# Kernel optimization log

Hardware: AMD Instinct MI355X
Metric: run time of the kernel (lower is better)

Reference implementation:

```python
import jax, jax.numpy as jnp
import numpy as np

SEQ, BATCH, D_MODEL, HEADS = 2048, 4, 1024, 16
D_K = D_MODEL // HEADS
SCALE = 1.0 / np.sqrt(D_K).astype(np.float32)


def setup_inputs() -> dict:
    key = jax.random.key(0)
    ks = jax.random.split(key, 12)
    s = 0.02
    inp = {
        "query": jax.random.normal(ks[0], (SEQ, BATCH, D_MODEL), jnp.float32),
        "key": jax.random.normal(ks[1], (SEQ, BATCH, D_MODEL), jnp.float32),
        "value": jax.random.normal(ks[2], (SEQ, BATCH, D_MODEL), jnp.float32),
        # causal mask [seq_q, seq_k, 1]; batch dim broadcasts per prepare_mask
        "mask": jnp.tril(jnp.ones((SEQ, SEQ), jnp.int32))[:, :, None],
        "Wq": jax.random.normal(ks[3], (D_MODEL, D_MODEL), jnp.float32) * s,
        "bq": jnp.zeros((D_MODEL,), jnp.float32),
        "Wk": jax.random.normal(ks[4], (D_MODEL, D_MODEL), jnp.float32) * s,
        "bk": jnp.zeros((D_MODEL,), jnp.float32),
        "Wv": jax.random.normal(ks[5], (D_MODEL, D_MODEL), jnp.float32) * s,
        "bv": jnp.zeros((D_MODEL,), jnp.float32),
        "Wo": jax.random.normal(ks[6], (D_MODEL, D_MODEL), jnp.float32) * s,
        "bo": jnp.zeros((D_MODEL,), jnp.float32),
    }
    return inp


def _heads(x, W, b):
    # [s, b, d_model] -> [s, b, h, d_k]
    y = jnp.einsum('sbd,de->sbe', x, W.T) + b
    return y.reshape(x.shape[0], x.shape[1], HEADS, D_K)


def reference(query, key, value, mask, Wq, bq, Wk, bk, Wv, bv, Wo, bo):
    seq_len, batch_size, _ = query.shape
    q = _heads(query, Wq, bq)
    k = _heads(key, Wk, bk)
    v = _heads(value, Wv, bv)
    # scores [i, j, b, h]
    scores = jnp.einsum('ibhd,jbhd->ijbh', q, k) * SCALE
    m = mask[:, :, :, None]  # [sq, sk, b_or_1, 1]
    scores = jnp.where(m == 0, jnp.float32(-jnp.inf), scores)
    attn = jax.nn.softmax(scores, axis=1)  # softmax over key dim j
    x = jnp.einsum('ijbh,jbhd->ibhd', attn, v)
    x = x.reshape(seq_len, batch_size, D_MODEL)
    return jnp.einsum('sbd,de->sbe', x, Wo.T) + bo
```

## Files before the change

### kernel.cpp

```cpp
#include <hip/hip_runtime.h>
#include <hip/hip_bf16.h>

#define SEQ 2048
#define BATCH 4
#define DM 1024
#define HEADS 16
#define DK 64
#define NBH 64
#define SC_LOG2E (0.125f * 1.4426950408889634f)

typedef unsigned short u16;
typedef __attribute__((ext_vector_type(8))) short bf16x8;
typedef __attribute__((ext_vector_type(4))) float f32x4;

__device__ inline u16 f2bf(float f) {
    unsigned int u = __builtin_bit_cast(unsigned int, f);
    u += 0x7fffu + ((u >> 16) & 1u);
    return (u16)(u >> 16);
}
__device__ inline float fexp2(float x) {
    float r; asm("v_exp_f32 %0, %1" : "=v"(r) : "v"(x)); return r;
}
__device__ inline unsigned pkbf(float a, float b) {
    unsigned r; asm("v_cvt_pk_bf16_f32 %0, %1, %2" : "=v"(r) : "v"(a), "v"(b)); return r;
}

__global__ __launch_bounds__(256)
void conv_w(const float* __restrict__ wq, const float* __restrict__ wk,
            const float* __restrict__ wv, const float* __restrict__ wo,
            u16* __restrict__ ow)
{
    const size_t W8 = (size_t)DM * DM / 8;
    size_t i = (size_t)blockIdx.x * 256 + threadIdx.x;
    int wsel = (int)(i >> 17);
    size_t off = i & (W8 - 1);
    const float* src = wsel == 0 ? wq : wsel == 1 ? wk : wsel == 2 ? wv : wo;
    u16* dst = ow + (size_t)wsel * DM * DM;
    float4 a = ((const float4*)src)[off * 2];
    float4 b = ((const float4*)src)[off * 2 + 1];
    uint4 w;
    w.x = pkbf(a.x, a.y); w.y = pkbf(a.z, a.w);
    w.z = pkbf(b.x, b.y); w.w = pkbf(b.z, b.w);
    *(uint4*)(dst + off * 8) = w;
}

__device__ inline void gstage(const u16* __restrict__ src, u16* dst,
                              int wave, int lane) {
    #pragma unroll
    for (int i = 0; i < 4; ++i) {
        int ci = (i * 4 + wave) * 64 + lane;
        int row = ci >> 3, ch = ci & 7;
        const u16* g = src + (size_t)row * 1024 + ((ch ^ (row & 7)) << 3);
        u16* l = dst + (i * 4 + wave) * 512;
        __builtin_amdgcn_global_load_lds(
            (const __attribute__((address_space(1))) unsigned int*)g,
            (__attribute__((address_space(3))) unsigned int*)l, 16, 0, 0);
    }
}
__device__ inline bf16x8 rdt(const u16* t, int row, int ch) {
    return *(const bf16x8*)(t + row * 64 + ((ch ^ (row & 7)) << 3));
}

__global__ __launch_bounds__(256, 2)
void gemm_bf(const u16* __restrict__ A, const u16* __restrict__ B,
             const float* __restrict__ bias, float* __restrict__ Out)
{
    __shared__ __align__(16) u16 sA[2][128 * 64];
    __shared__ __align__(16) u16 sB[2][128 * 64];
    const int tid  = threadIdx.x;
    const int lane = tid & 63, wave = tid >> 6;
    const int wr = (wave >> 1) * 64, wc = (wave & 1) * 64;
    const int l15 = lane & 15, lg = lane >> 4;
    const int row0 = blockIdx.x * 128, col0 = blockIdx.y * 128;
    const u16* Abase = A + (size_t)row0 * 1024;
    const u16* Bbase = B + (size_t)col0 * 1024;

    f32x4 acc[4][4];
    #pragma unroll
    for (int m = 0; m < 4; ++m)
        #pragma unroll
        for (int n = 0; n < 4; ++n) acc[m][n] = (f32x4){0.f, 0.f, 0.f, 0.f};

    gstage(Abase, sA[0], wave, lane);
    gstage(Bbase, sB[0], wave, lane);
    __syncthreads();

    int cur = 0;
    for (int kt = 0; kt < 16; ++kt) {
        if (kt < 15) {
            gstage(Abase + (kt + 1) * 64, sA[cur ^ 1], wave, lane);
            gstage(Bbase + (kt + 1) * 64, sB[cur ^ 1], wave, lane);
        }
        #pragma unroll
        for (int s = 0; s < 2; ++s) {
            bf16x8 af[4], bf[4];
            #pragma unroll
            for (int m = 0; m < 4; ++m)
                af[m] = rdt(sA[cur], wr + m * 16 + l15, s * 4 + lg);
            #pragma unroll
            for (int n = 0; n < 4; ++n)
                bf[n] = rdt(sB[cur], wc + n * 16 + l15, s * 4 + lg);
            __builtin_amdgcn_s_setprio(1);
            #pragma unroll
            for (int m = 0; m < 4; ++m)
                #pragma unroll
                for (int n = 0; n < 4; ++n)
                    acc[m][n] = __builtin_amdgcn_mfma_f32_16x16x32_bf16(
                        af[m], bf[n], acc[m][n], 0, 0, 0);
            __builtin_amdgcn_s_setprio(0);
        }
        __syncthreads();
        cur ^= 1;
    }
    #pragma unroll
    for (int m = 0; m < 4; ++m)
        #pragma unroll
        for (int n = 0; n < 4; ++n)
            #pragma unroll
            for (int r = 0; r < 4; ++r) {
                int R = row0 + wr + m * 16 + lg * 4 + r;
                int E = col0 + wc + n * 16 + l15;
                Out[(size_t)R * 1024 + E] = acc[m][n][r] + bias[E];
            }
}

__global__ __launch_bounds__(256, 2)
void gemm_qkv(const float* __restrict__ q, const float* __restrict__ k,
              const float* __restrict__ v, const u16* __restrict__ Wbf,
              const float* __restrict__ bq, const float* __restrict__ bk,
              const float* __restrict__ bv,
              u16* __restrict__ Qb, u16* __restrict__ Kb, u16* __restrict__ Vt)
{
    __shared__ __align__(16) u16 sA[2][128 * 64];
    __shared__ __align__(16) u16 sB[2][128 * 64];
    const int g = blockIdx.y >> 3;
    const float* A    = g == 0 ? q  : g == 1 ? k  : v;
    const float* bias = g == 0 ? bq : g == 1 ? bk : bv;
    u16* Out          = g == 0 ? Qb : g == 1 ? Kb : Vt;
    const u16* B = Wbf + (size_t)g * DM * DM;
    const float oscale = g == 0 ? SC_LOG2E : 1.0f;
    const bool vmode = (g == 2);

    const int tid  = threadIdx.x;
    const int lane = tid & 63, wave = tid >> 6;
    const int wr = (wave >> 1) * 64, wc = (wave & 1) * 64;
    const int l15 = lane & 15, lg = lane >> 4;
    const int row0 = blockIdx.x * 128, col0 = (blockIdx.y & 7) * 128;
    const int arow = tid >> 4;
    const int ach  = tid & 15;
    const float* Ag = A + (size_t)(row0 + arow) * 1024 + ach * 4;
    const u16* Bbase = B + (size_t)col0 * 1024;

    f32x4 acc[4][4];
    #pragma unroll
    for (int m = 0; m < 4; ++m)
        #pragma unroll
        for (int n = 0; n < 4; ++n) acc[m][n] = (f32x4){0.f, 0.f, 0.f, 0.f};

    auto loadA = [&](int kt, float4* r) {
        #pragma unroll
        for (int i = 0; i < 8; ++i)
            r[i] = *(const float4*)(Ag + (size_t)i * 16 * 1024 + kt * 64);
    };
    auto writeA = [&](const float4* r, u16* dst) {
        const int c16 = ach >> 1, half = ach & 1;
        #pragma unroll
        for (int i = 0; i < 8; ++i) {
            int row = arow + 16 * i;
            uint2 w;
            w.x = pkbf(r[i].x, r[i].y);
            w.y = pkbf(r[i].z, r[i].w);
            *(uint2*)(dst + row * 64 + ((c16 ^ (row & 7)) << 3) + half * 4) = w;
        }
    };

    {
        float4 a0[8];
        loadA(0, a0);
        gstage(Bbase, sB[0], wave, lane);
        writeA(a0, sA[0]);
    }
    __syncthreads();

    int cur = 0;
    for (int kt = 0; kt < 16; ++kt) {
        float4 an[8];
        const bool pre = (kt < 15);
        if (pre) {
            loadA(kt + 1, an);
            gstage(Bbase + (kt + 1) * 64, sB[cur ^ 1], wave, lane);
        }
        #pragma unroll
        for (int s = 0; s < 2; ++s) {
            bf16x8 af[4], bf[4];
            #pragma unroll
            for (int m = 0; m < 4; ++m)
                af[m] = rdt(sA[cur], wr + m * 16 + l15, s * 4 + lg);
            #pragma unroll
            for (int n = 0; n < 4; ++n)
                bf[n] = rdt(sB[cur], wc + n * 16 + l15, s * 4 + lg);
            __builtin_amdgcn_s_setprio(1);
            #pragma unroll
            for (int m = 0; m < 4; ++m)
                #pragma unroll
                for (int n = 0; n < 4; ++n)
                    acc[m][n] = __builtin_amdgcn_mfma_f32_16x16x32_bf16(
                        af[m], bf[n], acc[m][n], 0, 0, 0);
            __builtin_amdgcn_s_setprio(0);
        }
        if (pre) writeA(an, sA[cur ^ 1]);
        __syncthreads();
        cur ^= 1;
    }

    #pragma unroll
    for (int m = 0; m < 4; ++m)
        #pragma unroll
        for (int n = 0; n < 4; ++n)
            #pragma unroll
            for (int r = 0; r < 4; ++r) {
                int R = row0 + wr + m * 16 + lg * 4 + r;
                int E = col0 + wc + n * 16 + l15;
                float val = (acc[m][n][r] + bias[E]) * oscale;
                int s = R >> 2, b = R & 3, hh = E >> 6, d = E & 63;
                size_t idx = vmode
                    ? ((size_t)(b * HEADS + hh) * DK + d) * SEQ + s
                    : ((size_t)(b * HEADS + hh) * SEQ + s) * DK + d;
                Out[idx] = f2bf(val);
            }
}

__device__ inline void stage_tile(const u16* __restrict__ srcRow0, int srcStride,
                                  u16* tile, int wave, int lane) {
    #pragma unroll
    for (int i = 0; i < 2; ++i) {
        int row = wave * 16 + i * 8 + (lane >> 3);
        int chunk = (lane & 7) ^ (row & 7);
        const u16* g = srcRow0 + (size_t)row * srcStride + chunk * 8;
        u16* l = tile + (wave * 16 + i * 8) * 64;
        __builtin_amdgcn_global_load_lds(
            (const __attribute__((address_space(1))) unsigned int*)g,
            (__attribute__((address_space(3))) unsigned int*)l, 16, 0, 0);
    }
}
__device__ inline bf16x8 tread(const u16* tile, int row, int chunk) {
    return *(const bf16x8*)((const char*)tile + row * 128 + ((chunk ^ (row & 7)) << 4));
}

__global__ __launch_bounds__(256, 4)
void attn_fwd(const u16* __restrict__ Q, const u16* __restrict__ K,
              const u16* __restrict__ V, u16* __restrict__ X)
{
    __shared__ __align__(16) u16 sK[2][4096];
    __shared__ __align__(16) u16 sV[2][4096];
    __shared__ __align__(16) u16 plds[4][16 * 64];

    const int lin = blockIdx.x + 16 * blockIdx.y;
    const int xcd = lin & 7, ii = lin >> 3;
    const int bh  = (ii & 7) | (xcd << 3);
    const int tA  = ii >> 3;
    const int tB  = 31 - tA;
    const int b = bh >> 4, h = bh & 15;
    const int lane = threadIdx.x & 63, wave = threadIdx.x >> 6;
    const int l15 = lane & 15, lg = lane >> 4;
    const int qloc = wave * 16 + l15;
    const int swz = (l15 & 7) << 4;
    const u16* Qh = Q + (size_t)bh * SEQ * DK;
    const u16* Kh = K + (size_t)bh * SEQ * DK;
    const u16* Vh = V + (size_t)bh * SEQ * DK;

    const int qA = tA * 64 + wave * 16, qB = tB * 64 + wave * 16;
    const bf16x8 qfA0 = *(const bf16x8*)&Qh[(size_t)(qA + l15) * DK + lg * 8];
    const bf16x8 qfA1 = *(const bf16x8*)&Qh[(size_t)(qA + l15) * DK + 32 + lg * 8];
    const bf16x8 qfB0 = *(const bf16x8*)&Qh[(size_t)(qB + l15) * DK + lg * 8];
    const bf16x8 qfB1 = *(const bf16x8*)&Qh[(size_t)(qB + l15) * DK + 32 + lg * 8];

    f32x4 oA[4], oB[4];
    #pragma unroll
    for (int n = 0; n < 4; ++n) {
        oA[n] = (f32x4){0.f, 0.f, 0.f, 0.f};
        oB[n] = (f32x4){0.f, 0.f, 0.f, 0.f};
    }
    float lsA = 0.f, lsB = 0.f;
    u16* pw = &plds[wave][0];

    auto compute = [&](const u16* kt, const u16* vt,
                       const bf16x8& q0v, const bf16x8& q1v,
                       f32x4* o, float& ls, bool diag) {
        f32x4 sc[4];
        #pragma unroll
        for (int c = 0; c < 4; ++c) sc[c] = (f32x4){0.f, 0.f, 0.f, 0.f};

        __builtin_amdgcn_s_setprio(1);
        #pragma unroll
        for (int c = 0; c < 4; ++c) {
            bf16x8 k0 = tread(kt, 16 * c + l15, lg);
            bf16x8 k1 = tread(kt, 16 * c + l15, 4 + lg);
            sc[c] = __builtin_amdgcn_mfma_f32_16x16x32_bf16(k0, q0v, sc[c], 0, 0, 0);
            sc[c] = __builtin_amdgcn_mfma_f32_16x16x32_bf16(k1, q1v, sc[c], 0, 0, 0);
        }
        __builtin_amdgcn_s_setprio(0);

        #pragma unroll
        for (int c = 0; c < 4; ++c) {
            float p[4];
            #pragma unroll
            for (int r = 0; r < 4; ++r) {
                float e = fexp2(sc[c][r]);
                if (diag) {
                    int kl = 16 * c + 4 * lg + r;
                    e = (kl <= qloc) ? e : 0.f;
                }
                p[r] = e;
                ls += e;
            }
            uint2 w;
            w.x = pkbf(p[0], p[1]);
            w.y = pkbf(p[2], p[3]);
            *(uint2*)((char*)pw + l15 * 128 + ((32 * c + 8 * lg) ^ swz)) = w;
        }
        asm volatile("s_waitcnt lgkmcnt(0)" ::: "memory");
        __builtin_amdgcn_sched_barrier(0);
        bf16x8 pf0 = *(const bf16x8*)((const char*)pw + l15 * 128 + ((16 * lg) ^ swz));
        bf16x8 pf1 = *(const bf16x8*)((const char*)pw + l15 * 128 + ((64 + 16 * lg) ^ swz));

        __builtin_amdgcn_s_setprio(1);
        #pragma unroll
        for (int n = 0; n < 4; ++n) {
            bf16x8 v0 = tread(vt, 16 * n + l15, lg);
            bf16x8 v1 = tread(vt, 16 * n + l15, 4 + lg);
            o[n] = __builtin_amdgcn_mfma_f32_16x16x32_bf16(pf0, v0, o[n], 0, 0, 0);
            o[n] = __builtin_amdgcn_mfma_f32_16x16x32_bf16(pf1, v1, o[n], 0, 0, 0);
        }
        __builtin_amdgcn_s_setprio(0);
    };

    stage_tile(Kh, DK, sK[0], wave, lane);
    stage_tile(Vh, SEQ, sV[0], wave, lane);
    __syncthreads();

    const int nst = tB + 1;
    int cur = 0;
    for (int blk = 0; blk < nst; ++blk) {
        if (blk + 1 < nst) {
            stage_tile(Kh + (size_t)(blk + 1) * 64 * DK, DK, sK[cur ^ 1], wave, lane);
            stage_tile(Vh + (blk + 1) * 64, SEQ, sV[cur ^ 1], wave, lane);
        }
        if (blk <= tA)
            compute(sK[cur], sV[cur], qfA0, qfA1, oA, lsA, blk == tA);
        compute(sK[cur], sV[cur], qfB0, qfB1, oB, lsB, blk == tB);
        __syncthreads();
        cur ^= 1;
    }

    auto finish = [&](f32x4* o, float ls, int q0) {
        float tot = ls;
        tot += __shfl_xor(tot, 16, 64);
        tot += __shfl_xor(tot, 32, 64);
        float inv[4];
        #pragma unroll
        for (int r = 0; r < 4; ++r)
            inv[r] = 1.0f / __shfl(tot, lg * 4 + r, 64);
        #pragma unroll
        for (int n = 0; n < 4; ++n)
            #pragma unroll
            for (int r = 0; r < 4; ++r) {
                const int i = q0 + lg * 4 + r;
                X[((size_t)i * BATCH + b) * DM + h * DK + 16 * n + l15] =
                    f2bf(o[n][r] * inv[r]);
            }
    };
    finish(oA, lsA, qA);
    finish(oB, lsB, qB);
}

extern "C" void kernel_launch(void* const* d_in, const int* in_sizes, int n_in,
                              void* d_out, int out_size, void* d_ws, size_t ws_size,
                              hipStream_t stream) {
    const float* query = (const float*)d_in[0];
    const float* key   = (const float*)d_in[1];
    const float* value = (const float*)d_in[2];
    const float* Wq = (const float*)d_in[4];
    const float* bq = (const float*)d_in[5];
    const float* Wk = (const float*)d_in[6];
    const float* bk = (const float*)d_in[7];
    const float* Wv = (const float*)d_in[8];
    const float* bv = (const float*)d_in[9];
    const float* Wo = (const float*)d_in[10];
    const float* bo = (const float*)d_in[11];

    const size_t NELEM = (size_t)SEQ * BATCH * DM;
    const size_t WM    = (size_t)DM * DM;
    u16* Qb  = (u16*)d_ws;
    u16* Kb  = Qb + NELEM;
    u16* Vt  = Kb + NELEM;
    u16* Xb  = Vt + NELEM;
    u16* Wbf = Xb + NELEM;

    dim3 gb(256);
    hipLaunchKernelGGL(conv_w, dim3(2048), gb, 0, stream, Wq, Wk, Wv, Wo, Wbf);
    hipLaunchKernelGGL(gemm_qkv, dim3(64, 24), gb, 0, stream,
                       query, key, value, Wbf, bq, bk, bv, Qb, Kb, Vt);
    hipLaunchKernelGGL(attn_fwd, dim3(16, NBH), gb, 0, stream, Qb, Kb, Vt, Xb);
    hipLaunchKernelGGL(gemm_bf, dim3(64, 8), gb, 0, stream,
                       Xb, Wbf + 3 * WM, bo, (float*)d_out);
}
```

Before: 173.4 us.

## Split paired causal query tiles across 8 waves per attention block

The attention kernel now runs 512 threads per block. Waves 0-3 handle the short query tile tA and waves 4-7 handle the long tile tB, where before each of 4 waves processed both tiles serially. K/V staging is spread over 8 waves with one load each, and the P scratch buffer grows to 8 slots. This raises parallelism and cuts per-wave serial work and register pressure. The cost is that the tA waves sit idle at barriers once their causal range ends, which leaves the load unbalanced inside each block.

Result: slower. 185.4 us (+6.9%).

```diff
diff --git a/kernel.cpp b/kernel.cpp
--- a/kernel.cpp
+++ b/kernel.cpp
@@ -230,30 +230,27 @@
             }
 }
 
-__device__ inline void stage_tile(const u16* __restrict__ srcRow0, int srcStride,
-                                  u16* tile, int wave, int lane) {
-    #pragma unroll
-    for (int i = 0; i < 2; ++i) {
-        int row = wave * 16 + i * 8 + (lane >> 3);
-        int chunk = (lane & 7) ^ (row & 7);
-        const u16* g = srcRow0 + (size_t)row * srcStride + chunk * 8;
-        u16* l = tile + (wave * 16 + i * 8) * 64;
-        __builtin_amdgcn_global_load_lds(
-            (const __attribute__((address_space(1))) unsigned int*)g,
-            (__attribute__((address_space(3))) unsigned int*)l, 16, 0, 0);
-    }
+__device__ inline void stage_tile8(const u16* __restrict__ srcRow0, int srcStride,
+                                   u16* tile, int wave, int lane) {
+    int row = wave * 8 + (lane >> 3);
+    int chunk = (lane & 7) ^ (row & 7);
+    const u16* g = srcRow0 + (size_t)row * srcStride + chunk * 8;
+    u16* l = tile + wave * 512;
+    __builtin_amdgcn_global_load_lds(
+        (const __attribute__((address_space(1))) unsigned int*)g,
+        (__attribute__((address_space(3))) unsigned int*)l, 16, 0, 0);
 }
 __device__ inline bf16x8 tread(const u16* tile, int row, int chunk) {
     return *(const bf16x8*)((const char*)tile + row * 128 + ((chunk ^ (row & 7)) << 4));
 }
 
-__global__ __launch_bounds__(256, 4)
+__global__ __launch_bounds__(512, 6)
 void attn_fwd(const u16* __restrict__ Q, const u16* __restrict__ K,
               const u16* __restrict__ V, u16* __restrict__ X)
 {
     __shared__ __align__(16) u16 sK[2][4096];
     __shared__ __align__(16) u16 sV[2][4096];
-    __shared__ __align__(16) u16 plds[4][16 * 64];
+    __shared__ __align__(16) u16 plds[8][1024];
 
     const int lin = blockIdx.x + 16 * blockIdx.y;
     const int xcd = lin & 7, ii = lin >> 3;
@@ -262,31 +259,26 @@
     const int tB  = 31 - tA;
     const int b = bh >> 4, h = bh & 15;
     const int lane = threadIdx.x & 63, wave = threadIdx.x >> 6;
+    const int wq4 = wave & 3;
+    const int myT = (wave >> 2) ? tB : tA;
     const int l15 = lane & 15, lg = lane >> 4;
-    const int qloc = wave * 16 + l15;
+    const int qloc = wq4 * 16 + l15;
     const int swz = (l15 & 7) << 4;
     const u16* Qh = Q + (size_t)bh * SEQ * DK;
     const u16* Kh = K + (size_t)bh * SEQ * DK;
     const u16* Vh = V + (size_t)bh * SEQ * DK;
 
-    const int qA = tA * 64 + wave * 16, qB = tB * 64 + wave * 16;
-    const bf16x8 qfA0 = *(const bf16x8*)&Qh[(size_t)(qA + l15) * DK + lg * 8];
-    const bf16x8 qfA1 = *(const bf16x8*)&Qh[(size_t)(qA + l15) * DK + 32 + lg * 8];
-    const bf16x8 qfB0 = *(const bf16x8*)&Qh[(size_t)(qB + l15) * DK + lg * 8];
-    const bf16x8 qfB1 = *(const bf16x8*)&Qh[(size_t)(qB + l15) * DK + 32 + lg * 8];
-
-    f32x4 oA[4], oB[4];
-    #pragma unroll
-    for (int n = 0; n < 4; ++n) {
-        oA[n] = (f32x4){0.f, 0.f, 0.f, 0.f};
-        oB[n] = (f32x4){0.f, 0.f, 0.f, 0.f};
-    }
-    float lsA = 0.f, lsB = 0.f;
+    const int q0 = myT * 64 + wq4 * 16;
+    const bf16x8 qf0 = *(const bf16x8*)&Qh[(size_t)(q0 + l15) * DK + lg * 8];
+    const bf16x8 qf1 = *(const bf16x8*)&Qh[(size_t)(q0 + l15) * DK + 32 + lg * 8];
+
+    f32x4 o[4];
+    #pragma unroll
+    for (int n = 0; n < 4; ++n) o[n] = (f32x4){0.f, 0.f, 0.f, 0.f};
+    float ls = 0.f;
     u16* pw = &plds[wave][0];
 
-    auto compute = [&](const u16* kt, const u16* vt,
-                       const bf16x8& q0v, const bf16x8& q1v,
-                       f32x4* o, float& ls, bool diag) {
+    auto compute = [&](const u16* kt, const u16* vt, bool diag) {
         f32x4 sc[4];
         #pragma unroll
         for (int c = 0; c < 4; ++c) sc[c] = (f32x4){0.f, 0.f, 0.f, 0.f};
@@ -296,8 +288,8 @@
         for (int c = 0; c < 4; ++c) {
             bf16x8 k0 = tread(kt, 16 * c + l15, lg);
             bf16x8 k1 = tread(kt, 16 * c + l15, 4 + lg);
-            sc[c] = __builtin_amdgcn_mfma_f32_16x16x32_bf16(k0, q0v, sc[c], 0, 0, 0);
-            sc[c] = __builtin_amdgcn_mfma_f32_16x16x32_bf16(k1, q1v, sc[c], 0, 0, 0);
+            sc[c] = __builtin_amdgcn_mfma_f32_16x16x32_bf16(k0, qf0, sc[c], 0, 0, 0);
+            sc[c] = __builtin_amdgcn_mfma_f32_16x16x32_bf16(k1, qf1, sc[c], 0, 0, 0);
         }
         __builtin_amdgcn_s_setprio(0);
 
@@ -335,25 +327,24 @@
         __builtin_amdgcn_s_setprio(0);
     };
 
-    stage_tile(Kh, DK, sK[0], wave, lane);
-    stage_tile(Vh, SEQ, sV[0], wave, lane);
+    stage_tile8(Kh, DK, sK[0], wave, lane);
+    stage_tile8(Vh, SEQ, sV[0], wave, lane);
     __syncthreads();
 
     const int nst = tB + 1;
     int cur = 0;
     for (int blk = 0; blk < nst; ++blk) {
         if (blk + 1 < nst) {
-            stage_tile(Kh + (size_t)(blk + 1) * 64 * DK, DK, sK[cur ^ 1], wave, lane);
-            stage_tile(Vh + (blk + 1) * 64, SEQ, sV[cur ^ 1], wave, lane);
-        }
-        if (blk <= tA)
-            compute(sK[cur], sV[cur], qfA0, qfA1, oA, lsA, blk == tA);
-        compute(sK[cur], sV[cur], qfB0, qfB1, oB, lsB, blk == tB);
+            stage_tile8(Kh + (size_t)(blk + 1) * 64 * DK, DK, sK[cur ^ 1], wave, lane);
+            stage_tile8(Vh + (blk + 1) * 64, SEQ, sV[cur ^ 1], wave, lane);
+        }
+        if (blk <= myT)
+            compute(sK[cur], sV[cur], blk == myT);
         __syncthreads();
         cur ^= 1;
     }
 
-    auto finish = [&](f32x4* o, float ls, int q0) {
+    {
         float tot = ls;
         tot += __shfl_xor(tot, 16, 64);
         tot += __shfl_xor(tot, 32, 64);
@@ -369,9 +360,7 @@
                 X[((size_t)i * BATCH + b) * DM + h * DK + 16 * n + l15] =
                     f2bf(o[n][r] * inv[r]);
             }
-    };
-    finish(oA, lsA, qA);
-    finish(oB, lsB, qB);
+    }
 }
 
 extern "C" void kernel_launch(void* const* d_in, const int* in_sizes, int n_in,
@@ -401,7 +390,7 @@
     hipLaunchKernelGGL(conv_w, dim3(2048), gb, 0, stream, Wq, Wk, Wv, Wo, Wbf);
     hipLaunchKernelGGL(gemm_qkv, dim3(64, 24), gb, 0, stream,
                        query, key, value, Wbf, bq, bk, bv, Qb, Kb, Vt);
-    hipLaunchKernelGGL(attn_fwd, dim3(16, NBH), gb, 0, stream, Qb, Kb, Vt, Xb);
+    hipLaunchKernelGGL(attn_fwd, dim3(16, NBH), dim3(512), 0, stream, Qb, Kb, Vt, Xb);
     hipLaunchKernelGGL(gemm_bf, dim3(64, 8), gb, 0, stream,
                        Xb, Wbf + 3 * WM, bo, (float*)d_out);
 }
```
